# Kernel tuning notes

Measured on AMD Instinct MI355X. Metric: run time of the kernel, lower is better.

## Reference

```python
import jax, jax.numpy as jnp
import numpy as np

D_MODEL = 2048
EXPAND = 2
INNER = EXPAND * D_MODEL          # 4096
HEADDIM = 64
NHEADS = INNER // HEADDIM         # 64
D_CONV = 4
BATCH, SEQLEN = 2, 4096


def setup_inputs() -> dict:
    key = jax.random.key(0)
    ks = jax.random.split(key, 12)
    f32 = jnp.float32
    return {
        "hidden_states": jax.random.normal(ks[0], (BATCH, SEQLEN, D_MODEL), f32),
        "in_proj_w": jax.random.normal(ks[1], (INNER, D_MODEL), f32) * 0.02,
        "gate_proj_w": jax.random.normal(ks[2], (INNER, D_MODEL), f32) * 0.02,
        "out_proj_w": jax.random.normal(ks[3], (D_MODEL, INNER), f32) * 0.02,
        "conv_weight": jax.random.normal(ks[4], (INNER, D_CONV), f32) * 0.02,
        "conv_bias": jnp.zeros((INNER,), f32),
        "dt_w": jax.random.normal(ks[5], (NHEADS, HEADDIM), f32) * 0.02,
        "dt_b": jnp.zeros((NHEADS,), f32),
        "A_log": jax.random.normal(ks[6], (NHEADS, HEADDIM), f32) * 0.1,
        "B": jax.random.normal(ks[7], (NHEADS, HEADDIM), f32) * 0.02,
        "C": jax.random.normal(ks[8], (NHEADS, HEADDIM), f32) * 0.02,
        "D": jnp.ones((NHEADS, HEADDIM), f32),
    }


def _dw_causal_conv_silu(x, w, b):
    # x: (B, L, C), w: (C, K), b: (C,). Causal depthwise conv + SiLU.
    K = w.shape[1]
    L = x.shape[1]
    xp = jnp.pad(x, ((0, 0), (K - 1, 0), (0, 0)))
    y = b
    for k in range(K):  # K=4, tiny fixed loop
        y = y + w[:, k] * xp[:, k:k + L, :]
    return jax.nn.silu(y)


def _diag_ssm_scan(a, u):
    # Linear recurrence s_t = a_t * s_{t-1} + u_t along axis=1 (seqlen).
    def comb(c1, c2):
        a1, b1 = c1
        a2, b2 = c2
        return a1 * a2, a2 * b1 + b2
    _, s = jax.lax.associative_scan(comb, (a, u), axis=1)
    return s


def reference(hidden_states, in_proj_w, gate_proj_w, out_proj_w,
              conv_weight, conv_bias, dt_w, dt_b, A_log, B, C, D):
    batch, seqlen, _ = hidden_states.shape
    projected = jnp.einsum('bld,cd->blc', hidden_states, in_proj_w)
    conv_out = _dw_causal_conv_silu(projected, conv_weight, conv_bias)
    gate = jax.nn.sigmoid(jnp.einsum('bld,cd->blc', hidden_states, gate_proj_w))

    X = conv_out.reshape(batch, seqlen, NHEADS, HEADDIM)
    dt = jax.nn.softplus(jnp.einsum('blhp,hp->blh', X, dt_w) + dt_b)  # (b,l,h)
    A = -jnp.exp(A_log)                                               # (h,p)

    a = jnp.exp(dt[..., None] * A)          # (b,l,h,p) decay factors
    u = dt[..., None] * B * X               # (b,l,h,p) driven input
    s = _diag_ssm_scan(a, u)                # (b,l,h,p) states
    y = C * s + D * X                       # (b,l,h,p)

    combined = y.reshape(batch, seqlen, INNER) * gate
    return jnp.einsum('blc,dc->bld', combined, out_proj_w)
```

## Files before the change

kernel.cpp:

```cpp
#include <hip/hip_runtime.h>
#include <cstdint>
#include <cstddef>

typedef unsigned short ushort;
typedef unsigned int uint;
typedef __attribute__((ext_vector_type(8))) short short8;
typedef __attribute__((ext_vector_type(8))) unsigned short ushort8;
typedef __attribute__((ext_vector_type(4))) float float4v;

#define DM    2048
#define INNERC 4096
#define LSEQ  4096
#define NBATCH 2
#define MROWS 8192
#define NHH   64
#define HDD   64
#define NCHUNK 32
#define CHLEN  128
#define CROWS 8

__device__ __forceinline__ float bf2f(ushort u) {
    return __uint_as_float(((unsigned int)u) << 16);
}
__device__ __forceinline__ ushort f2bf(float f) {
    unsigned int u = __float_as_uint(f);
    unsigned int r = u + 0x7FFFu + ((u >> 16) & 1u);
    return (ushort)(r >> 16);
}

__device__ __forceinline__ void async_cp16(const ushort* __restrict__ g, ushort* l) {
    __builtin_amdgcn_global_load_lds(
        (const __attribute__((address_space(1))) unsigned int*)g,
        (__attribute__((address_space(3))) unsigned int*)l,
        16, 0, 0);
}

__global__ void diag_kernel(float* __restrict__ out, float val) {
    if (threadIdx.x == 0 && blockIdx.x == 0) out[0] = val;
}

__global__ __launch_bounds__(256) void cast_bf16_kernel(
    const float* __restrict__ in, ushort* __restrict__ out, int n) {
    const int i = (blockIdx.x * 256 + threadIdx.x) * 8;
    if (i + 8 > n) return;
    const float4v a = *(const float4v*)(in + i);
    const float4v b = *(const float4v*)(in + i + 4);
    ushort8 o;
    o[0] = f2bf(a[0]); o[1] = f2bf(a[1]); o[2] = f2bf(a[2]); o[3] = f2bf(a[3]);
    o[4] = f2bf(b[0]); o[5] = f2bf(b[1]); o[6] = f2bf(b[2]); o[7] = f2bf(b[3]);
    *(ushort8*)(out + i) = o;
}


#define PH_PRE() do { \
    __builtin_amdgcn_s_barrier(); \
    asm volatile("s_waitcnt lgkmcnt(0)"); } while (0)

#define PH_POST() do { \
    __builtin_amdgcn_s_barrier(); } while (0)

#define MFMA_Q(AF, RBASE, CL) do { \
    __builtin_amdgcn_s_setprio(1); \
    _Pragma("unroll") for (int kk = 0; kk < 2; ++kk) \
    _Pragma("unroll") for (int rm = 0; rm < 4; ++rm) \
    _Pragma("unroll") for (int cn = 0; cn < 2; ++cn) \
        acc[(RBASE) + rm][(CL) + cn] = __builtin_amdgcn_mfma_f32_16x16x32_bf16( \
            AF[rm][kk], bf[(CL) + cn][kk], acc[(RBASE) + rm][(CL) + cn], 0, 0, 0); \
    __builtin_amdgcn_s_setprio(0); } while (0)

#define READ_A(DST, BUF, HB) do { \
    _Pragma("unroll") for (int rm = 0; rm < 4; ++rm) { \
        DST[rm][0] = *(const short8*)&As[BUF][offA_k0 + ((HB) * 4 + rm) * 1024]; \
        DST[rm][1] = *(const short8*)&As[BUF][offA_k1 + ((HB) * 4 + rm) * 1024]; \
    } } while (0)

#define READ_B2(BUF, CNLO) do { \
    _Pragma("unroll") for (int cn = 0; cn < 2; ++cn) { \
        bf[(CNLO) + cn][0] = *(const short8*)&Bs[BUF][offB_k0 + ((CNLO) + cn) * 1024]; \
        bf[(CNLO) + cn][1] = *(const short8*)&Bs[BUF][offB_k1 + ((CNLO) + cn) * 1024]; \
    } } while (0)

#define STAGE(G, OFF, LBASE) do { \
    async_cp16((G) + (OFF),       (LBASE) + (tid << 3)); \
    async_cp16((G) + (OFF) + k64, (LBASE) + (tid << 3) + 4096); \
    (OFF) += 64; } while (0)

template <int EPI>
__global__ __launch_bounds__(512, 2) void gemm256(
    const ushort* __restrict__ Ab, const ushort* __restrict__ Wb,
    void* __restrict__ Out, const ushort* __restrict__ Aux,
    int M, int N, int K) {
    __shared__ ushort As[2][16384];
    __shared__ ushort Bs[2][16384];

    const int tid  = threadIdx.x;
    const int lane = tid & 63;
    const int w    = tid >> 6;
    const int wm   = w >> 2;
    const int wn   = w & 3;
    const int l15  = lane & 15;
    const int l4   = lane >> 4;
    const int swz7 = l15 & 7;
    const int s01  = swz7 & 3;
    const int b2   = (swz7 >> 2) & 1;

    const int gx   = gridDim.x;
    const int nwg  = gx * gridDim.y;
    const int orig = blockIdx.y * gx + blockIdx.x;
    const int swz  = (orig & 7) * (nwg >> 3) + (orig >> 3);
    const int row0 = (swz / gx) * 256;
    const int col0 = (swz % gx) * 256;

    const int ni = K >> 7;

    const int commA   = (wm * 128 + l15) * 64 + (l4 ^ s01) * 8;
    const int offA_k0 = commA + (b2 ? 32 : 0);
    const int offA_k1 = commA + (b2 ? 0 : 32);
    const int commB   = (wn * 64 + l15) * 64 + (l4 ^ s01) * 8;
    const int offB_k0 = commB + (b2 ? 32 : 0);
    const int offB_k1 = commB + (b2 ? 0 : 32);

    const uint rr8 = (uint)(tid >> 3);
    const uint kg8 = (uint)(((tid & 7) ^ ((tid >> 3) & 7)) * 8);
    const uint k64 = (uint)64 * (uint)K;
    uint oA0 = (uint)(row0) * (uint)K + rr8 * (uint)K + kg8;
    uint oA1 = oA0 + (uint)128 * (uint)K;
    uint oW0 = (uint)(col0) * (uint)K + rr8 * (uint)K + kg8;
    uint oW1 = oW0 + (uint)128 * (uint)K;

    float4v acc[8][4];
#pragma unroll
    for (int i2 = 0; i2 < 8; i2++)
#pragma unroll
        for (int j2 = 0; j2 < 4; j2++) {
            float4v z = {0.f, 0.f, 0.f, 0.f};
            acc[i2][j2] = z;
        }

    short8 afL[4][2], afH[4][2], bf[4][2];

    STAGE(Ab, oA0, &As[0][0]);
    STAGE(Ab, oA1, &As[0][8192]);
    STAGE(Wb, oW0, &Bs[0][0]);
    STAGE(Wb, oW1, &Bs[0][8192]);
    STAGE(Ab, oA0, &As[1][0]);
    STAGE(Ab, oA1, &As[1][8192]);
    STAGE(Wb, oW0, &Bs[1][0]);
    STAGE(Wb, oW1, &Bs[1][8192]);
    asm volatile("s_waitcnt vmcnt(8)" ::: "memory");
    __builtin_amdgcn_s_barrier();

#pragma unroll 1
    for (int i = 0; i < ni - 1; ++i) {
        READ_A(afL, 0, 0);
        READ_B2(0, 0);
        asm volatile("s_waitcnt lgkmcnt(8)");
        PH_PRE();
        MFMA_Q(afL, 0, 0);
        PH_POST();

        READ_B2(0, 2);
        PH_PRE();
        MFMA_Q(afL, 0, 2);
        PH_POST();

        READ_A(afH, 0, 1);
        STAGE(Wb, oW0, &Bs[0][0]);
        PH_PRE();
        MFMA_Q(afH, 4, 2);
        PH_POST();

        STAGE(Wb, oW1, &Bs[0][8192]);
        PH_PRE();
        MFMA_Q(afH, 4, 0);
        asm volatile("s_waitcnt vmcnt(4)" ::: "memory");
        __builtin_amdgcn_s_barrier();

        READ_A(afL, 1, 0);
        READ_B2(1, 0);
        STAGE(Ab, oA0, &As[0][0]);
        asm volatile("s_waitcnt lgkmcnt(8)");
        PH_PRE();
        MFMA_Q(afL, 0, 0);
        PH_POST();

        READ_B2(1, 2);
        STAGE(Ab, oA1, &As[0][8192]);
        PH_PRE();
        MFMA_Q(afL, 0, 2);
        PH_POST();

        READ_A(afH, 1, 1);
        STAGE(Wb, oW0, &Bs[1][0]);
        STAGE(Wb, oW1, &Bs[1][8192]);
        PH_PRE();
        MFMA_Q(afH, 4, 2);
        PH_POST();

        STAGE(Ab, oA0, &As[1][0]);
        STAGE(Ab, oA1, &As[1][8192]);
        PH_PRE();
        MFMA_Q(afH, 4, 0);
        asm volatile("s_waitcnt vmcnt(8)" ::: "memory");
        __builtin_amdgcn_s_barrier();
    }

    {
        READ_A(afL, 0, 0);
        READ_B2(0, 0);
        READ_B2(0, 2);
        READ_A(afH, 0, 1);
        __builtin_amdgcn_s_setprio(1);
        MFMA_Q(afL, 0, 0);
        MFMA_Q(afL, 0, 2);
        MFMA_Q(afH, 4, 2);
        MFMA_Q(afH, 4, 0);
        __builtin_amdgcn_s_setprio(0);
        asm volatile("s_waitcnt vmcnt(0)" ::: "memory");
        __builtin_amdgcn_s_barrier();
        READ_A(afL, 1, 0);
        READ_B2(1, 0);
        READ_B2(1, 2);
        READ_A(afH, 1, 1);
        __builtin_amdgcn_s_setprio(1);
        MFMA_Q(afL, 0, 0);
        MFMA_Q(afL, 0, 2);
        MFMA_Q(afH, 4, 2);
        MFMA_Q(afH, 4, 0);
        __builtin_amdgcn_s_setprio(0);
    }

#pragma unroll
    for (int rm = 0; rm < 8; ++rm) {
#pragma unroll
        for (int cn = 0; cn < 4; ++cn) {
            const int r0 = row0 + wm * 128 + rm * 16 + l4 * 4;
            const int cc = col0 + wn * 64 + cn * 16 + l15;
#pragma unroll
            for (int rr = 0; rr < 4; ++rr) {
                const float v = acc[rm][cn][rr];
                const size_t off = (size_t)(r0 + rr) * N + cc;
                if (EPI == 0) {
                    ((ushort*)Out)[off] = f2bf(v);
                } else if (EPI == 1) {
                    const float g = 1.0f / (1.0f + __expf(-v));
                    ((ushort*)Out)[off] = f2bf(g * bf2f(Aux[off]));
                } else {
                    ((float*)Out)[off] = v;
                }
            }
        }
    }
}

__global__ __launch_bounds__(256) void conv_silu_kernel(
    const ushort* __restrict__ proj, const float* __restrict__ cw,
    const float* __restrict__ cb, const float* __restrict__ dtw,
    const float* __restrict__ dtb, ushort* __restrict__ X,
    float* __restrict__ dt) {
    const int blk  = blockIdx.x;
    const int half = blk & 1;
    const int tile = blk >> 1;
    const int bl0  = tile * CROWS;
    const bool atStart = ((bl0 & (LSEQ - 1)) == 0);
    const int c0 = half * 2048 + threadIdx.x * 8;
    const int h  = c0 >> 6;

    float4v w[8];
    const float4v* wp4 = (const float4v*)(cw + (size_t)c0 * 4);
#pragma unroll
    for (int t = 0; t < 8; t++) w[t] = wp4[t];
    float bias[8];
    const float4v b0 = *(const float4v*)(cb + c0);
    const float4v b1 = *(const float4v*)(cb + c0 + 4);
#pragma unroll
    for (int t = 0; t < 4; t++) { bias[t] = b0[t]; bias[t + 4] = b1[t]; }

    float dtwv[8];
    const float4v d0 = *(const float4v*)(dtw + c0);
    const float4v d1 = *(const float4v*)(dtw + c0 + 4);
#pragma unroll
    for (int t = 0; t < 4; t++) { dtwv[t] = d0[t]; dtwv[t + 4] = d1[t]; }
    const float dtbv = dtb[h];

    const size_t base = (size_t)bl0 * INNERC + c0;
    ushort8 w0, w1, w2;
    const ushort8 zz = {0, 0, 0, 0, 0, 0, 0, 0};
    if (atStart) {
        w0 = zz; w1 = zz; w2 = zz;
    } else {
        w0 = *(const ushort8*)(proj + base - 3 * (size_t)INNERC);
        w1 = *(const ushort8*)(proj + base - 2 * (size_t)INNERC);
        w2 = *(const ushort8*)(proj + base - 1 * (size_t)INNERC);
    }
#pragma unroll
    for (int r = 0; r < CROWS; r++) {
        const ushort8 cur = *(const ushort8*)(proj + base + (size_t)r * INNERC);
        ushort8 o;
        float dacc = 0.0f;
#pragma unroll
        for (int j = 0; j < 8; j++) {
            const float acc = bias[j]
                + w[j][0] * bf2f(w0[j]) + w[j][1] * bf2f(w1[j])
                + w[j][2] * bf2f(w2[j]) + w[j][3] * bf2f(cur[j]);
            const float s = acc / (1.0f + __expf(-acc));
            o[j] = f2bf(s);
            dacc += s * dtwv[j];
        }
        *(ushort8*)(X + base + (size_t)r * INNERC) = o;
        dacc += __shfl_xor(dacc, 1, 64);
        dacc += __shfl_xor(dacc, 2, 64);
        dacc += __shfl_xor(dacc, 4, 64);
        if ((threadIdx.x & 7) == 0) {
            const float z = dacc + dtbv;
            dt[(bl0 + r) * 64 + h] = (z > 20.0f) ? z : __logf(1.0f + __expf(z));
        }
        w0 = w1; w1 = w2; w2 = cur;
    }
}

__global__ __launch_bounds__(256) void scan_pass1(
    const ushort* __restrict__ X, const float* __restrict__ dt,
    const float* __restrict__ A_log, const float* __restrict__ Bv,
    float* __restrict__ sumP, float* __restrict__ sumS) {
    const int task = blockIdx.x * 4 + (threadIdx.x >> 6);
    const int p  = threadIdx.x & 63;
    const int ch = task & (NCHUNK - 1);
    const int bh = task >> 5;
    const int h  = bh & 63;
    const int b  = bh >> 6;
    const float Ac = -__expf(A_log[h * 64 + p]);
    const float Bc = Bv[h * 64 + p];
    float Pr = 1.0f, s = 0.0f;
    const int bl0 = b * LSEQ + ch * CHLEN;
#pragma unroll 4
    for (int i = 0; i < CHLEN; i++) {
        const int bl   = bl0 + i;
        const float dtv = dt[bl * 64 + h];
        const float x   = bf2f(X[(size_t)bl * INNERC + h * 64 + p]);
        const float a   = __expf(dtv * Ac);
        Pr *= a;
        s = a * s + dtv * Bc * x;
    }
    sumP[(size_t)task * 64 + p] = Pr;
    sumS[(size_t)task * 64 + p] = s;
}

__global__ __launch_bounds__(64) void scan_pass2(
    const float* __restrict__ sumP, const float* __restrict__ sumS,
    float* __restrict__ carry) {
    const int bh = blockIdx.x;
    const int p  = threadIdx.x;
    float c = 0.0f;
    for (int ch = 0; ch < NCHUNK; ch++) {
        const size_t idx = ((size_t)bh * NCHUNK + ch) * 64 + p;
        carry[idx] = c;
        c = sumP[idx] * c + sumS[idx];
    }
}

__global__ __launch_bounds__(256) void scan_pass3(
    const ushort* __restrict__ X, const float* __restrict__ dt,
    const float* __restrict__ carry,
    const float* __restrict__ A_log, const float* __restrict__ Bv,
    const float* __restrict__ Cv, const float* __restrict__ Dv,
    ushort* __restrict__ Y) {
    const int task = blockIdx.x * 4 + (threadIdx.x >> 6);
    const int p  = threadIdx.x & 63;
    const int ch = task & (NCHUNK - 1);
    const int bh = task >> 5;
    const int h  = bh & 63;
    const int b  = bh >> 6;
    const float Ac = -__expf(A_log[h * 64 + p]);
    const float Bc = Bv[h * 64 + p];
    const float Cc = Cv[h * 64 + p];
    const float Dc = Dv[h * 64 + p];
    float s = carry[(size_t)task * 64 + p];
    const int bl0 = b * LSEQ + ch * CHLEN;
#pragma unroll 2
    for (int i = 0; i < CHLEN; i++) {
        const int bl = bl0 + i;
        const size_t xoff = (size_t)bl * INNERC + h * 64 + p;
        const float dtv = dt[bl * 64 + h];
        const float x   = bf2f(X[xoff]);
        const float a   = __expf(dtv * Ac);
        s = a * s + dtv * Bc * x;
        Y[xoff] = f2bf(Cc * s + Dc * x);
    }
}

#define OFF_PROJ  ((size_t)0)
#define OFF_HID   ((size_t)67108864)
#define OFF_WB    ((size_t)100663296)
#define OFF_DT    ((size_t)117440512)
#define OFF_SUMP  ((size_t)119537664)
#define OFF_SUMS  ((size_t)120586240)
#define OFF_CARRY ((size_t)121634816)
#define WS_NEEDED ((size_t)122683392)

extern "C" void kernel_launch(void* const* d_in, const int* in_sizes, int n_in,
                              void* d_out, int out_size, void* d_ws, size_t ws_size,
                              hipStream_t stream) {
    if (ws_size < WS_NEEDED) {
        diag_kernel<<<1, 64, 0, stream>>>((float*)d_out, (float)(ws_size >> 20));
        return;
    }
    const float* hidden = (const float*)d_in[0];
    const float* w_in   = (const float*)d_in[1];
    const float* w_gate = (const float*)d_in[2];
    const float* w_out  = (const float*)d_in[3];
    const float* conv_w = (const float*)d_in[4];
    const float* conv_b = (const float*)d_in[5];
    const float* dt_w   = (const float*)d_in[6];
    const float* dt_b   = (const float*)d_in[7];
    const float* A_log  = (const float*)d_in[8];
    const float* Bv     = (const float*)d_in[9];
    const float* Cv     = (const float*)d_in[10];
    const float* Dv     = (const float*)d_in[11];

    char* ws = (char*)d_ws;
    ushort* projbuf = (ushort*)(ws + OFF_PROJ);
    ushort* hid16   = (ushort*)(ws + OFF_HID);
    ushort* wbuf    = (ushort*)(ws + OFF_WB);
    float*  dtf     = (float*)(ws + OFF_DT);
    float*  sumP    = (float*)(ws + OFF_SUMP);
    float*  sumS    = (float*)(ws + OFF_SUMS);
    float*  carry   = (float*)(ws + OFF_CARRY);
    ushort* x16     = (ushort*)d_out;

    cast_bf16_kernel<<<8192, 256, 0, stream>>>(hidden, hid16, MROWS * DM);
    cast_bf16_kernel<<<4096, 256, 0, stream>>>(w_in, wbuf, INNERC * DM);

    gemm256<0><<<dim3(INNERC / 256, MROWS / 256), 512, 0, stream>>>(
        hid16, wbuf, projbuf, nullptr, MROWS, INNERC, DM);

    conv_silu_kernel<<<(MROWS / CROWS) * 2, 256, 0, stream>>>(
        projbuf, conv_w, conv_b, dt_w, dt_b, x16, dtf);

    scan_pass1<<<(NBATCH * NHH * NCHUNK) / 4, 256, 0, stream>>>(
        x16, dtf, A_log, Bv, sumP, sumS);
    scan_pass2<<<NBATCH * NHH, 64, 0, stream>>>(sumP, sumS, carry);
    scan_pass3<<<(NBATCH * NHH * NCHUNK) / 4, 256, 0, stream>>>(
        x16, dtf, carry, A_log, Bv, Cv, Dv, projbuf);

    cast_bf16_kernel<<<4096, 256, 0, stream>>>(w_gate, wbuf, INNERC * DM);
    gemm256<1><<<dim3(INNERC / 256, MROWS / 256), 512, 0, stream>>>(
        hid16, wbuf, projbuf, projbuf, MROWS, INNERC, DM);

    cast_bf16_kernel<<<4096, 256, 0, stream>>>(w_out, wbuf, DM * INNERC);
    gemm256<2><<<dim3(DM / 256, MROWS / 256), 512, 0, stream>>>(
        projbuf, wbuf, d_out, nullptr, MROWS, DM, INNERC);
}
```

Measured before the change: 647.5 us.

## Fuse conv+SiLU with scan pass1, merge input casts, drop GEMM lgkmcnt wait

```diff
diff --git a/kernel.cpp b/kernel.cpp
--- a/kernel.cpp
+++ b/kernel.cpp
@@ -17,7 +17,6 @@
 #define HDD   64
 #define NCHUNK 32
 #define CHLEN  128
-#define CROWS 8
 
 __device__ __forceinline__ float bf2f(ushort u) {
     return __uint_as_float(((unsigned int)u) << 16);
@@ -51,13 +50,30 @@
     *(ushort8*)(out + i) = o;
 }
 
-
-#define PH_PRE() do { \
-    __builtin_amdgcn_s_barrier(); \
-    asm volatile("s_waitcnt lgkmcnt(0)"); } while (0)
-
-#define PH_POST() do { \
-    __builtin_amdgcn_s_barrier(); } while (0)
+__global__ __launch_bounds__(256) void cast2_bf16_kernel(
+    const float* __restrict__ in1, ushort* __restrict__ out1, int n1,
+    const float* __restrict__ in2, ushort* __restrict__ out2, int n2) {
+    int i = (blockIdx.x * 256 + threadIdx.x) * 8;
+    const float* in;
+    ushort* out;
+    if (i < n1) {
+        in = in1 + i; out = out1 + i;
+    } else {
+        const int j = i - n1;
+        if (j + 8 > n2) return;
+        in = in2 + j; out = out2 + j;
+    }
+    const float4v a = *(const float4v*)(in);
+    const float4v b = *(const float4v*)(in + 4);
+    ushort8 o;
+    o[0] = f2bf(a[0]); o[1] = f2bf(a[1]); o[2] = f2bf(a[2]); o[3] = f2bf(a[3]);
+    o[4] = f2bf(b[0]); o[5] = f2bf(b[1]); o[6] = f2bf(b[2]); o[7] = f2bf(b[3]);
+    *(ushort8*)(out) = o;
+}
+
+
+#define PH_PRE() __builtin_amdgcn_s_barrier()
+#define PH_POST() __builtin_amdgcn_s_barrier()
 
 #define MFMA_Q(AF, RBASE, CL) do { \
     __builtin_amdgcn_s_setprio(1); \
@@ -253,97 +269,69 @@
     }
 }
 
-__global__ __launch_bounds__(256) void conv_silu_kernel(
+#define CSCH 256
+__global__ __launch_bounds__(256) void conv_scan1_kernel(
     const ushort* __restrict__ proj, const float* __restrict__ cw,
     const float* __restrict__ cb, const float* __restrict__ dtw,
-    const float* __restrict__ dtb, ushort* __restrict__ X,
-    float* __restrict__ dt) {
-    const int blk  = blockIdx.x;
-    const int half = blk & 1;
-    const int tile = blk >> 1;
-    const int bl0  = tile * CROWS;
-    const bool atStart = ((bl0 & (LSEQ - 1)) == 0);
-    const int c0 = half * 2048 + threadIdx.x * 8;
-    const int h  = c0 >> 6;
-
-    float4v w[8];
-    const float4v* wp4 = (const float4v*)(cw + (size_t)c0 * 4);
-#pragma unroll
-    for (int t = 0; t < 8; t++) w[t] = wp4[t];
-    float bias[8];
-    const float4v b0 = *(const float4v*)(cb + c0);
-    const float4v b1 = *(const float4v*)(cb + c0 + 4);
-#pragma unroll
-    for (int t = 0; t < 4; t++) { bias[t] = b0[t]; bias[t + 4] = b1[t]; }
-
-    float dtwv[8];
-    const float4v d0 = *(const float4v*)(dtw + c0);
-    const float4v d1 = *(const float4v*)(dtw + c0 + 4);
-#pragma unroll
-    for (int t = 0; t < 4; t++) { dtwv[t] = d0[t]; dtwv[t + 4] = d1[t]; }
-    const float dtbv = dtb[h];
-
-    const size_t base = (size_t)bl0 * INNERC + c0;
-    ushort8 w0, w1, w2;
-    const ushort8 zz = {0, 0, 0, 0, 0, 0, 0, 0};
-    if (atStart) {
-        w0 = zz; w1 = zz; w2 = zz;
+    const float* __restrict__ dtb, const float* __restrict__ A_log,
+    const float* __restrict__ Bv, ushort* __restrict__ X,
+    float* __restrict__ dt, float* __restrict__ sumP,
+    float* __restrict__ sumS) {
+    const int blk   = blockIdx.x;
+    const int slice = blk & 15;
+    const int chunk = blk >> 4;
+    const int b     = chunk >> 5;
+    const int chk   = chunk & 31;
+    const int bl0   = b * LSEQ + chk * CHLEN;
+    const int c     = slice * CSCH + threadIdx.x;
+    const int h     = c >> 6;
+    const int p     = c & 63;
+    const int lane  = threadIdx.x & 63;
+
+    const float4v wv   = *(const float4v*)(cw + (size_t)c * 4);
+    const float biasv  = cb[c];
+    const float dtwv   = dtw[c];
+    const float dtbv   = dtb[h];
+    const float Ac     = -__expf(A_log[c]);
+    const float Bc     = Bv[c];
+
+    const size_t base = (size_t)bl0 * INNERC + c;
+    float f0, f1, f2;
+    if (chk == 0) {
+        f0 = 0.f; f1 = 0.f; f2 = 0.f;
     } else {
-        w0 = *(const ushort8*)(proj + base - 3 * (size_t)INNERC);
-        w1 = *(const ushort8*)(proj + base - 2 * (size_t)INNERC);
-        w2 = *(const ushort8*)(proj + base - 1 * (size_t)INNERC);
-    }
-#pragma unroll
-    for (int r = 0; r < CROWS; r++) {
-        const ushort8 cur = *(const ushort8*)(proj + base + (size_t)r * INNERC);
-        ushort8 o;
-        float dacc = 0.0f;
-#pragma unroll
-        for (int j = 0; j < 8; j++) {
-            const float acc = bias[j]
-                + w[j][0] * bf2f(w0[j]) + w[j][1] * bf2f(w1[j])
-                + w[j][2] * bf2f(w2[j]) + w[j][3] * bf2f(cur[j]);
-            const float s = acc / (1.0f + __expf(-acc));
-            o[j] = f2bf(s);
-            dacc += s * dtwv[j];
-        }
-        *(ushort8*)(X + base + (size_t)r * INNERC) = o;
-        dacc += __shfl_xor(dacc, 1, 64);
-        dacc += __shfl_xor(dacc, 2, 64);
-        dacc += __shfl_xor(dacc, 4, 64);
-        if ((threadIdx.x & 7) == 0) {
-            const float z = dacc + dtbv;
-            dt[(bl0 + r) * 64 + h] = (z > 20.0f) ? z : __logf(1.0f + __expf(z));
-        }
-        w0 = w1; w1 = w2; w2 = cur;
-    }
-}
-
-__global__ __launch_bounds__(256) void scan_pass1(
-    const ushort* __restrict__ X, const float* __restrict__ dt,
-    const float* __restrict__ A_log, const float* __restrict__ Bv,
-    float* __restrict__ sumP, float* __restrict__ sumS) {
-    const int task = blockIdx.x * 4 + (threadIdx.x >> 6);
-    const int p  = threadIdx.x & 63;
-    const int ch = task & (NCHUNK - 1);
-    const int bh = task >> 5;
-    const int h  = bh & 63;
-    const int b  = bh >> 6;
-    const float Ac = -__expf(A_log[h * 64 + p]);
-    const float Bc = Bv[h * 64 + p];
+        f0 = bf2f(proj[base - 3 * (size_t)INNERC]);
+        f1 = bf2f(proj[base - 2 * (size_t)INNERC]);
+        f2 = bf2f(proj[base - 1 * (size_t)INNERC]);
+    }
+
     float Pr = 1.0f, s = 0.0f;
-    const int bl0 = b * LSEQ + ch * CHLEN;
 #pragma unroll 4
-    for (int i = 0; i < CHLEN; i++) {
-        const int bl   = bl0 + i;
-        const float dtv = dt[bl * 64 + h];
-        const float x   = bf2f(X[(size_t)bl * INNERC + h * 64 + p]);
-        const float a   = __expf(dtv * Ac);
-        Pr *= a;
-        s = a * s + dtv * Bc * x;
-    }
-    sumP[(size_t)task * 64 + p] = Pr;
-    sumS[(size_t)task * 64 + p] = s;
+    for (int r = 0; r < CHLEN; ++r) {
+        const float fc = bf2f(proj[base + (size_t)r * INNERC]);
+        const float a4 = biasv + wv[0] * f0 + wv[1] * f1 + wv[2] * f2 + wv[3] * fc;
+        const float sl = a4 / (1.0f + __expf(-a4));
+        const ushort xb = f2bf(sl);
+        X[base + (size_t)r * INNERC] = xb;
+        float d = sl * dtwv;
+        d += __shfl_xor(d, 1, 64);
+        d += __shfl_xor(d, 2, 64);
+        d += __shfl_xor(d, 4, 64);
+        d += __shfl_xor(d, 8, 64);
+        d += __shfl_xor(d, 16, 64);
+        d += __shfl_xor(d, 32, 64);
+        const float z   = d + dtbv;
+        const float dtv = (z > 20.0f) ? z : __logf(1.0f + __expf(z));
+        if (lane == 0) dt[(bl0 + r) * 64 + h] = dtv;
+        const float xr = bf2f(xb);
+        const float aa = __expf(dtv * Ac);
+        Pr *= aa;
+        s = aa * s + dtv * Bc * xr;
+        f0 = f1; f1 = f2; f2 = fc;
+    }
+    const size_t task = (size_t)((b * 64 + h) * 32 + chk);
+    sumP[task * 64 + p] = Pr;
+    sumS[task * 64 + p] = s;
 }
 
 __global__ __launch_bounds__(64) void scan_pass2(
@@ -428,17 +416,15 @@
     float*  carry   = (float*)(ws + OFF_CARRY);
     ushort* x16     = (ushort*)d_out;
 
-    cast_bf16_kernel<<<8192, 256, 0, stream>>>(hidden, hid16, MROWS * DM);
-    cast_bf16_kernel<<<4096, 256, 0, stream>>>(w_in, wbuf, INNERC * DM);
+    cast2_bf16_kernel<<<12288, 256, 0, stream>>>(
+        hidden, hid16, MROWS * DM, w_in, wbuf, INNERC * DM);
 
     gemm256<0><<<dim3(INNERC / 256, MROWS / 256), 512, 0, stream>>>(
         hid16, wbuf, projbuf, nullptr, MROWS, INNERC, DM);
 
-    conv_silu_kernel<<<(MROWS / CROWS) * 2, 256, 0, stream>>>(
-        projbuf, conv_w, conv_b, dt_w, dt_b, x16, dtf);
-
-    scan_pass1<<<(NBATCH * NHH * NCHUNK) / 4, 256, 0, stream>>>(
-        x16, dtf, A_log, Bv, sumP, sumS);
+    conv_scan1_kernel<<<(INNERC / CSCH) * (NBATCH * NCHUNK), 256, 0, stream>>>(
+        projbuf, conv_w, conv_b, dt_w, dt_b, A_log, Bv, x16, dtf, sumP, sumS);
+
     scan_pass2<<<NBATCH * NHH, 64, 0, stream>>>(sumP, sumS, carry);
     scan_pass3<<<(NBATCH * NHH * NCHUNK) / 4, 256, 0, stream>>>(
         x16, dtf, carry, A_log, Bv, Cv, Dv, projbuf);
```

Measured after the change: 695.4 us. +7.4%, slower.
